# Optimization experiments

Hardware: AMD Instinct MI355X
Metric: run time of the kernel (lower is better)

The kernel has to match this reference:

```python
import jax, jax.numpy as jnp
import numpy as np

BETA = 0.001  # commitment loss weight from __init__ default


def setup_inputs() -> dict:
    key = jax.random.key(0)
    k1, k2 = jax.random.split(key)
    N, INPUT_DIM = 8192, 1024
    S, K, D = 32, 1024, 32  # nsplits, num_embeddings, embedding_dim
    z = jax.random.normal(k1, (N, INPUT_DIM), dtype=jnp.float32)
    # Stacked codebook weights: one [K, D] embedding table per split.
    W = jax.random.normal(k2, (S, K, D), dtype=jnp.float32)
    return {"z": z, "W": W}


def reference(z, W):
    N, INPUT_DIM = z.shape
    S, K, D = W.shape
    zc = z.reshape(N, S, D)  # per-split chunks, matches torch.chunk(z, S, -1)
    # Squared euclidean distances ||z||^2 + ||w||^2 - 2 z.w  -> [N, S, K]
    d2 = (
        jnp.sum(zc * zc, axis=-1, keepdims=True)
        + jnp.sum(W * W, axis=-1)[None, :, :]
        - 2.0 * jnp.einsum("nsd,skd->nsk", zc, W)
    )
    idx = jnp.argmin(d2, axis=-1)  # [N, S]
    # Gather nearest codes: W[s, idx[n, s]] -> [N, S, D]
    zq = W[jnp.arange(S)[None, :], idx]
    # Sum over splits of per-split mse means; equal split sizes so this is
    # S * mean over the whole tensor.
    sg = jax.lax.stop_gradient
    loss = S * (
        jnp.mean((sg(zq) - zc) ** 2) + BETA * jnp.mean((zq - sg(zc)) ** 2)
    )
    # Straight-through estimator
    zq_st = zc + sg(zq - zc)
    return zq_st.reshape(N, INPUT_DIM), loss
```

## Files before the change

### kernel.cpp

```cpp
#include <hip/hip_runtime.h>
#include <math.h>

#define NN 8192
#define SS 32
#define DD 32
#define KK 1024
#define OUT_ELEMS ((size_t)NN * SS * DD)

#define LOSS_SCALE (32.0f * 1.001f / 8388608.0f)

typedef _Float16 half8 __attribute__((ext_vector_type(8)));
typedef float   floatx4 __attribute__((ext_vector_type(4)));

#define CH_TILES 8
#define CHUNK_K  (CH_TILES * 16)
#define NCHUNK   (KK / CHUNK_K)
#define RG 2
#define WAVES 8
#define BLK_ROWS (WAVES * RG * 16)
#define NBLOCKS ((NN / BLK_ROWS) * SS)


#define W2P_OFF  4096
#define WHP_OFF  (W2P_OFF + SS * KK * 4)
#define WLP_OFF  (WHP_OFF + SS * KK * DD * 2)

typedef const __attribute__((address_space(1))) void* gas_p;
typedef __attribute__((address_space(3))) void* las_p;

__device__ __forceinline__ void gll16(const void* g, void* l) {
    __builtin_amdgcn_global_load_lds((gas_p)g, (las_p)l, 16, 0, 0);
}
__device__ __forceinline__ void gll4(const void* g, void* l) {
    __builtin_amdgcn_global_load_lds((gas_p)g, (las_p)l, 4, 0, 0);
}

__global__ __launch_bounds__(256) void w_pre(const float* __restrict__ W,
                                             _Float16* __restrict__ WhP,
                                             _Float16* __restrict__ WlP,
                                             float* __restrict__ w2P) {
    const int u    = blockIdx.x * 256 + threadIdx.x;
    const int s    = u >> 12;
    const int g    = (u >> 6) & 63;
    const int l    = u & 63;
    const int col  = l & 15;
    const int quad = l >> 4;
    const int k    = g * 16 + col;
    const float* src = W + ((size_t)s * KK + k) * DD + quad * 8;
    const float4 va = ((const float4*)src)[0];
    const float4 vb = ((const float4*)src)[1];
    const float v[8] = {va.x, va.y, va.z, va.w, vb.x, vb.y, vb.z, vb.w};
    half8 h8, l8; float ps = 0.0f;
    #pragma unroll
    for (int j = 0; j < 8; ++j) {
        const float x = v[j];
        ps = fmaf(x, x, ps);
        const _Float16 h = (_Float16)x;
        h8[j] = h;
        l8[j] = (_Float16)(x - (float)h);
    }
    ps += __shfl_xor(ps, 16, 64);
    ps += __shfl_xor(ps, 32, 64);
    *(half8*)(WhP + (size_t)u * 8) = h8;
    *(half8*)(WlP + (size_t)u * 8) = l8;
    if (quad == 0) w2P[s * KK + k] = ps;
}

__global__ __launch_bounds__(512, 4) void vq_fused(const float* __restrict__ z,
                                                   const float* __restrict__ W,
                                                   const _Float16* __restrict__ WhP,
                                                   const _Float16* __restrict__ WlP,
                                                   const float* __restrict__ w2P,
                                                   float* __restrict__ out,
                                                   float* __restrict__ part) {
    __shared__ _Float16 bufH[2][CH_TILES][64][8];
    __shared__ _Float16 bufL[2][CH_TILES][64][8];
    __shared__ float    w2b[2][CHUNK_K];
    __shared__ int      lds_idx[WAVES][32];
    __shared__ float    lds_part[WAVES];

    const int s    = blockIdx.x & (SS - 1);
    const int n0b  = (blockIdx.x >> 5) * BLK_ROWS;
    const int tid  = threadIdx.x;
    const int wv   = tid >> 6;
    const int lane = tid & 63;
    const int col  = lane & 15;
    const int quad = lane >> 4;

    const float* __restrict__ Ws = W + (size_t)s * KK * DD;
    const int n0w = n0b + wv * (RG * 16);

    half8 zh[RG], zl[RG];
    #pragma unroll
    for (int rg = 0; rg < RG; ++rg) {
        const float* zp = z + (size_t)(n0w + rg * 16 + col) * (SS * DD) + s * DD + quad * 8;
        const float4 va = ((const float4*)zp)[0];
        const float4 vb = ((const float4*)zp)[1];
        const float src[8] = {va.x, va.y, va.z, va.w, vb.x, vb.y, vb.z, vb.w};
        #pragma unroll
        for (int j = 0; j < 8; ++j) {
            const float v = -2.0f * src[j];
            const _Float16 h = (_Float16)v;
            zh[rg][j] = h;
            zl[rg][j] = (_Float16)(v - (float)h);
        }
    }

    floatx4 best[RG];
    int bi[RG][4];
    #pragma unroll
    for (int rg = 0; rg < RG; ++rg) {
        best[rg] = (floatx4){INFINITY, INFINITY, INFINITY, INFINITY};
        bi[rg][0] = bi[rg][1] = bi[rg][2] = bi[rg][3] = 0;
    }

    const _Float16* whs = WhP + (size_t)s * 64 * 512 + (size_t)lane * 8;
    const _Float16* wls = WlP + (size_t)s * 64 * 512 + (size_t)lane * 8;
    const float*    w2s = w2P + (size_t)s * KK + lane;

    auto stage = [&](int c, int nb) {
        const size_t t = (size_t)c * CH_TILES + wv;
        gll16(whs + t * 512, &bufH[nb][wv][0][0]);
        gll16(wls + t * 512, &bufL[nb][wv][0][0]);
        if (wv < 2) gll4(w2s + c * CHUNK_K + wv * 64, &w2b[nb][wv * 64]);
    };

    stage(0, 0);
    __syncthreads();

    for (int c = 0; c < NCHUNK; ++c) {
        const int b = c & 1;
        if (c + 1 < NCHUNK) stage(c + 1, b ^ 1);

        half8 bh = *(const half8*)&bufH[b][0][lane][0];
        half8 bl = *(const half8*)&bufL[b][0][lane][0];
        float w2v = w2b[b][col];
        #pragma unroll
        for (int tt = 0; tt < CH_TILES; ++tt) {
            half8 nbh = bh, nbl = bl; float nw2 = w2v;
            if (tt + 1 < CH_TILES) {
                nbh = *(const half8*)&bufH[b][tt + 1][lane][0];
                nbl = *(const half8*)&bufL[b][tt + 1][lane][0];
                nw2 = w2b[b][(tt + 1) * 16 + col];
            }
            const floatx4 c0 = {w2v, w2v, w2v, w2v};
            const int tk = c * CH_TILES + tt;
            __builtin_amdgcn_s_setprio(1);
            floatx4 a0 = __builtin_amdgcn_mfma_f32_16x16x32_f16(zh[0], bh, c0, 0, 0, 0);
            floatx4 a1 = __builtin_amdgcn_mfma_f32_16x16x32_f16(zh[1], bh, c0, 0, 0, 0);
            a0 = __builtin_amdgcn_mfma_f32_16x16x32_f16(zl[0], bh, a0, 0, 0, 0);
            a1 = __builtin_amdgcn_mfma_f32_16x16x32_f16(zl[1], bh, a1, 0, 0, 0);
            a0 = __builtin_amdgcn_mfma_f32_16x16x32_f16(zh[0], bl, a0, 0, 0, 0);
            a1 = __builtin_amdgcn_mfma_f32_16x16x32_f16(zh[1], bl, a1, 0, 0, 0);
            __builtin_amdgcn_s_setprio(0);
            #pragma unroll
            for (int i = 0; i < 4; ++i) {
                if (a0[i] < best[0][i]) { best[0][i] = a0[i]; bi[0][i] = tk; }
                if (a1[i] < best[1][i]) { best[1][i] = a1[i]; bi[1][i] = tk; }
            }
            bh = nbh; bl = nbl; w2v = nw2;
        }
        if (c + 1 < NCHUNK) __syncthreads();
    }

    #pragma unroll
    for (int rg = 0; rg < RG; ++rg) {
        #pragma unroll
        for (int i = 0; i < 4; ++i) {
            float v = best[rg][i];
            int   k = bi[rg][i] * 16 + col;
            #pragma unroll
            for (int m = 1; m < 16; m <<= 1) {
                const float vo = __shfl_xor(v, m, 64);
                const int   ko = __shfl_xor(k, m, 64);
                if (vo < v || (vo == v && ko < k)) { v = vo; k = ko; }
            }
            if (col == 0) lds_idx[wv][rg * 16 + quad * 4 + i] = k;
        }
    }
    __syncthreads();

    const int r  = lane & 31;
    const int dh = (lane >> 5) * 16;
    const int krow = lds_idx[wv][r];
    const float* wsrc = Ws + (size_t)krow * DD + dh;
    const size_t zoff = (size_t)(n0w + r) * (SS * DD) + s * DD + dh;
    const float* zsrc = z + zoff;
    float* od = out + zoff;
    float sq = 0.0f;
    #pragma unroll
    for (int cc = 0; cc < 4; ++cc) {
        const float4 wq = ((const float4*)wsrc)[cc];
        const float4 zv = ((const float4*)zsrc)[cc];
        const float d0 = wq.x - zv.x, d1 = wq.y - zv.y;
        const float d2 = wq.z - zv.z, d3 = wq.w - zv.w;
        sq = fmaf(d0, d0, sq); sq = fmaf(d1, d1, sq);
        sq = fmaf(d2, d2, sq); sq = fmaf(d3, d3, sq);
        ((float4*)od)[cc] = wq;
    }
    #pragma unroll
    for (int off = 32; off > 0; off >>= 1) sq += __shfl_down(sq, off, 64);

    if (lane == 0) lds_part[wv] = sq;
    __syncthreads();
    if (tid == 0) {
        float t = 0.0f;
        #pragma unroll
        for (int w = 0; w < WAVES; ++w) t += lds_part[w];
        part[blockIdx.x] = t;
    }
}

__global__ __launch_bounds__(256) void vq_loss(const float* __restrict__ part,
                                               float* __restrict__ out) {
    __shared__ float l[4];
    const int tid = threadIdx.x;
    float sum = 0.0f;
    #pragma unroll
    for (int i = 0; i < NBLOCKS / 256; ++i) sum += part[tid + i * 256];
    #pragma unroll
    for (int off = 32; off > 0; off >>= 1) sum += __shfl_down(sum, off, 64);
    if ((tid & 63) == 0) l[tid >> 6] = sum;
    __syncthreads();
    if (tid == 0) out[OUT_ELEMS] = (l[0] + l[1] + l[2] + l[3]) * LOSS_SCALE;
}

extern "C" void kernel_launch(void* const* d_in, const int* in_sizes, int n_in,
                              void* d_out, int out_size, void* d_ws, size_t ws_size,
                              hipStream_t stream) {
    const float* z = (const float*)d_in[0];
    const float* W = (const float*)d_in[1];
    float* out  = (float*)d_out;

    char* ws = (char*)d_ws;
    float*    part = (float*)ws;
    float*    w2P  = (float*)(ws + W2P_OFF);
    _Float16* WhP  = (_Float16*)(ws + WHP_OFF);
    _Float16* WlP  = (_Float16*)(ws + WLP_OFF);

    w_pre<<<dim3(512), dim3(256), 0, stream>>>(W, WhP, WlP, w2P);
    vq_fused<<<dim3(NBLOCKS), dim3(512), 0, stream>>>(z, W, WhP, WlP, w2P, out, part);
    vq_loss<<<dim3(1), dim3(256), 0, stream>>>(part, out);
}
```

Baseline: 149.6 us.

## Load whole per-split codebook into LDS once and double block size

Replaces the double-buffered chunked streaming of the fp16 hi/lo codebook with a single upfront load of the entire split's codebook (about 129KB of LDS) and one barrier. Blocks grow to 16 waves (1024 threads), halving the grid and doubling reuse of each LDS-staged codebook. This removes the per-chunk barriers, but LDS use now limits occupancy to about one block per CU and there is no overlap between the initial load and compute. The hidden epilogue, which sizes things by WAVES, must handle 16 waves.

```diff
diff --git a/kernel.cpp b/kernel.cpp
--- a/kernel.cpp
+++ b/kernel.cpp
@@ -12,11 +12,9 @@
 typedef _Float16 half8 __attribute__((ext_vector_type(8)));
 typedef float   floatx4 __attribute__((ext_vector_type(4)));
 
-#define CH_TILES 8
-#define CHUNK_K  (CH_TILES * 16)
-#define NCHUNK   (KK / CHUNK_K)
+#define NTILES 64
 #define RG 2
-#define WAVES 8
+#define WAVES 16
 #define BLK_ROWS (WAVES * RG * 16)
 #define NBLOCKS ((NN / BLK_ROWS) * SS)
 
@@ -66,16 +64,16 @@
     if (quad == 0) w2P[s * KK + k] = ps;
 }
 
-__global__ __launch_bounds__(512, 4) void vq_fused(const float* __restrict__ z,
-                                                   const float* __restrict__ W,
-                                                   const _Float16* __restrict__ WhP,
-                                                   const _Float16* __restrict__ WlP,
-                                                   const float* __restrict__ w2P,
-                                                   float* __restrict__ out,
-                                                   float* __restrict__ part) {
-    __shared__ _Float16 bufH[2][CH_TILES][64][8];
-    __shared__ _Float16 bufL[2][CH_TILES][64][8];
-    __shared__ float    w2b[2][CHUNK_K];
+__global__ __launch_bounds__(1024, 4) void vq_fused(const float* __restrict__ z,
+                                                    const float* __restrict__ W,
+                                                    const _Float16* __restrict__ WhP,
+                                                    const _Float16* __restrict__ WlP,
+                                                    const float* __restrict__ w2P,
+                                                    float* __restrict__ out,
+                                                    float* __restrict__ part) {
+    __shared__ _Float16 bufH[NTILES][64][8];
+    __shared__ _Float16 bufL[NTILES][64][8];
+    __shared__ float    w2b[KK];
     __shared__ int      lds_idx[WAVES][32];
     __shared__ float    lds_part[WAVES];
 
@@ -90,6 +88,22 @@
     const float* __restrict__ Ws = W + (size_t)s * KK * DD;
     const int n0w = n0b + wv * (RG * 16);
 
+    {
+        const char* gH = (const char*)(WhP + (size_t)s * (NTILES * 512));
+        const char* gL = (const char*)(WlP + (size_t)s * (NTILES * 512));
+        char* lH = (char*)&bufH[0][0][0];
+        char* lL = (char*)&bufL[0][0][0];
+        const int wvB = wv * 1024;
+        #pragma unroll
+        for (int i = 0; i < 4; ++i) {
+            const int off = i * 16384 + wvB;
+            gll16(gH + off + lane * 16, lH + off);
+            gll16(gL + off + lane * 16, lL + off);
+        }
+        const float* g2 = w2P + (size_t)s * KK + wv * 64;
+        gll4(g2 + lane, (char*)w2b + wv * 256);
+    }
+
     half8 zh[RG], zl[RG];
     #pragma unroll
     for (int rg = 0; rg < RG; ++rg) {
@@ -114,53 +128,27 @@
         bi[rg][0] = bi[rg][1] = bi[rg][2] = bi[rg][3] = 0;
     }
 
-    const _Float16* whs = WhP + (size_t)s * 64 * 512 + (size_t)lane * 8;
-    const _Float16* wls = WlP + (size_t)s * 64 * 512 + (size_t)lane * 8;
-    const float*    w2s = w2P + (size_t)s * KK + lane;
-
-    auto stage = [&](int c, int nb) {
-        const size_t t = (size_t)c * CH_TILES + wv;
-        gll16(whs + t * 512, &bufH[nb][wv][0][0]);
-        gll16(wls + t * 512, &bufL[nb][wv][0][0]);
-        if (wv < 2) gll4(w2s + c * CHUNK_K + wv * 64, &w2b[nb][wv * 64]);
-    };
-
-    stage(0, 0);
-    __syncthreads();
-
-    for (int c = 0; c < NCHUNK; ++c) {
-        const int b = c & 1;
-        if (c + 1 < NCHUNK) stage(c + 1, b ^ 1);
-
-        half8 bh = *(const half8*)&bufH[b][0][lane][0];
-        half8 bl = *(const half8*)&bufL[b][0][lane][0];
-        float w2v = w2b[b][col];
-        #pragma unroll
-        for (int tt = 0; tt < CH_TILES; ++tt) {
-            half8 nbh = bh, nbl = bl; float nw2 = w2v;
-            if (tt + 1 < CH_TILES) {
-                nbh = *(const half8*)&bufH[b][tt + 1][lane][0];
-                nbl = *(const half8*)&bufL[b][tt + 1][lane][0];
-                nw2 = w2b[b][(tt + 1) * 16 + col];
-            }
-            const floatx4 c0 = {w2v, w2v, w2v, w2v};
-            const int tk = c * CH_TILES + tt;
-            __builtin_amdgcn_s_setprio(1);
-            floatx4 a0 = __builtin_amdgcn_mfma_f32_16x16x32_f16(zh[0], bh, c0, 0, 0, 0);
-            floatx4 a1 = __builtin_amdgcn_mfma_f32_16x16x32_f16(zh[1], bh, c0, 0, 0, 0);
-            a0 = __builtin_amdgcn_mfma_f32_16x16x32_f16(zl[0], bh, a0, 0, 0, 0);
-            a1 = __builtin_amdgcn_mfma_f32_16x16x32_f16(zl[1], bh, a1, 0, 0, 0);
-            a0 = __builtin_amdgcn_mfma_f32_16x16x32_f16(zh[0], bl, a0, 0, 0, 0);
-            a1 = __builtin_amdgcn_mfma_f32_16x16x32_f16(zh[1], bl, a1, 0, 0, 0);
-            __builtin_amdgcn_s_setprio(0);
-            #pragma unroll
-            for (int i = 0; i < 4; ++i) {
-                if (a0[i] < best[0][i]) { best[0][i] = a0[i]; bi[0][i] = tk; }
-                if (a1[i] < best[1][i]) { best[1][i] = a1[i]; bi[1][i] = tk; }
-            }
-            bh = nbh; bl = nbl; w2v = nw2;
-        }
-        if (c + 1 < NCHUNK) __syncthreads();
+    __syncthreads();
+
+    #pragma unroll 8
+    for (int tt = 0; tt < NTILES; ++tt) {
+        const half8 bh = *(const half8*)&bufH[tt][lane][0];
+        const half8 bl = *(const half8*)&bufL[tt][lane][0];
+        const float w2v = w2b[tt * 16 + col];
+        const floatx4 c0 = {w2v, w2v, w2v, w2v};
+        __builtin_amdgcn_s_setprio(1);
+        floatx4 a0 = __builtin_amdgcn_mfma_f32_16x16x32_f16(zh[0], bh, c0, 0, 0, 0);
+        floatx4 a1 = __builtin_amdgcn_mfma_f32_16x16x32_f16(zh[1], bh, c0, 0, 0, 0);
+        a0 = __builtin_amdgcn_mfma_f32_16x16x32_f16(zl[0], bh, a0, 0, 0, 0);
+        a1 = __builtin_amdgcn_mfma_f32_16x16x32_f16(zl[1], bh, a1, 0, 0, 0);
+        a0 = __builtin_amdgcn_mfma_f32_16x16x32_f16(zh[0], bl, a0, 0, 0, 0);
+        a1 = __builtin_amdgcn_mfma_f32_16x16x32_f16(zh[1], bl, a1, 0, 0, 0);
+        __builtin_amdgcn_s_setprio(0);
+        #pragma unroll
+        for (int i = 0; i < 4; ++i) {
+            if (a0[i] < best[0][i]) { best[0][i] = a0[i]; bi[0][i] = tt; }
+            if (a1[i] < best[1][i]) { best[1][i] = a1[i]; bi[1][i] = tt; }
+        }
     }
 
     #pragma unroll
@@ -239,6 +227,6 @@
     _Float16* WlP  = (_Float16*)(ws + WLP_OFF);
 
     w_pre<<<dim3(512), dim3(256), 0, stream>>>(W, WhP, WlP, w2P);
-    vq_fused<<<dim3(NBLOCKS), dim3(512), 0, stream>>>(z, W, WhP, WlP, w2P, out, part);
+    vq_fused<<<dim3(NBLOCKS), dim3(1024), 0, stream>>>(z, W, WhP, WlP, w2P, out, part);
     vq_loss<<<dim3(1), dim3(256), 0, stream>>>(part, out);
 }
```

Result: slower. 157.3 us (+5.1%).
